# Kernel optimization log

Measured on AMD Instinct MI355X. Metric: run time of the kernel, lower is better.

## Reference

```python
import jax, jax.numpy as jnp
import numpy as np

B, T, D, H, L = 8192, 80, 32, 64, 3


def setup_inputs() -> dict:
    key = jax.random.key(0)
    ks = jax.random.split(key, 16)
    s = lambda k, shape, fan: jax.random.normal(k, shape, jnp.float32) / np.sqrt(fan)
    inp = {"x": jax.random.normal(ks[0], (B, T, D), jnp.float32)}
    dims_in = [D, H, H]
    i = 1
    for l in range(L):
        din = dims_in[l]
        inp[f"W_ih{l}"] = s(ks[i], (H, din), H); i += 1
        inp[f"W_hh{l}"] = s(ks[i], (H, H), H); i += 1
        inp[f"b_ih{l}"] = s(ks[i], (H,), H); i += 1
        inp[f"b_hh{l}"] = s(ks[i], (H,), H); i += 1
    inp["W_fc"] = s(ks[i], (1, H), H); i += 1
    inp["b_fc"] = s(ks[i], (1,), H)
    return inp


def _rnn_layer(xs, W_ih, W_hh, b_ih, b_hh):
    # xs: [T, B, Din] -> ys: [T, B, H]; tanh RNN recurrence (PyTorch nn.RNN math)
    pre = jnp.einsum('tbd,hd->tbh', xs, W_ih) + b_ih + b_hh  # input proj precomputed
    h0 = jnp.zeros((xs.shape[1], W_hh.shape[0]), xs.dtype)
    def step(h, p):
        h_new = jnp.tanh(p + h @ W_hh.T)
        return h_new, h_new
    _, ys = jax.lax.scan(step, h0, pre)
    return ys


def reference(x, W_ih0, W_hh0, b_ih0, b_hh0, W_ih1, W_hh1, b_ih1, b_hh1,
              W_ih2, W_hh2, b_ih2, b_hh2, W_fc, b_fc):
    # x: [B, T, D] (batch_first) -> time-major [T, B, D]
    h = jnp.swapaxes(x, 0, 1)
    params = [(W_ih0, W_hh0, b_ih0, b_hh0),
              (W_ih1, W_hh1, b_ih1, b_hh1),
              (W_ih2, W_hh2, b_ih2, b_hh2)]
    for (W_ih, W_hh, b_ih, b_hh) in params:
        h = _rnn_layer(h, W_ih, W_hh, b_ih, b_hh)
    last = h[-1]                      # [B, H] == out[:, -1, :]
    return last @ W_fc.T + b_fc       # [B, 1]
```

## Files before the change

### kernel.cpp

```cpp
#include <hip/hip_runtime.h>
#include <hip/hip_bf16.h>
#include <cstddef>


typedef __attribute__((ext_vector_type(8))) short s16x8;
typedef __attribute__((ext_vector_type(4))) short s16x4;
typedef __attribute__((ext_vector_type(4))) float fx4;

#define MFMA32(A, B, C) __builtin_amdgcn_mfma_f32_16x16x32_bf16((A), (B), (C), 0, 0, 0)

#if __has_builtin(__builtin_amdgcn_exp2f)
#define EXP2F(x) __builtin_amdgcn_exp2f(x)
#else
#define EXP2F(x) exp2f(x)
#endif
#if __has_builtin(__builtin_amdgcn_rcpf)
#define RCPF(x) __builtin_amdgcn_rcpf(x)
#else
#define RCPF(x) (1.0f / (x))
#endif

static constexpr float K2LOG2E = 2.8853900817779268f;

__device__ __forceinline__ short f2bf(float f) {
  union { float f; unsigned u; } v; v.f = f;
  unsigned r = v.u + 0x7FFFu + ((v.u >> 16) & 1u);
  return (short)(r >> 16);
}
__device__ __forceinline__ float bf2f(short s) {
  union { unsigned u; float f; } v; v.u = ((unsigned)(unsigned short)s) << 16;
  return v.f;
}
__device__ __forceinline__ unsigned pk2bf(float a, float b) {
  float2 t; t.x = a; t.y = b;
  union { __hip_bfloat162 h; unsigned u; } c;
  c.h = __float22bfloat162_rn(t);
  return c.u;
}

__device__ __forceinline__ s16x8 wfragA32(const float* W, int ncols, int row, int col0) {
  const float* p = W + row * ncols + col0;
  s16x8 r;
#pragma unroll
  for (int i = 0; i < 8; ++i) r[i] = f2bf(p[i]);
  return r;
}

__device__ __forceinline__ s16x8 wfragWhh32(const float* W, int row, int q, int h) {
  const float* p = W + row * 64 + 32 * h + 4 * q;
  s16x8 r;
#pragma unroll
  for (int i = 0; i < 4; ++i) r[i] = f2bf(p[i]);
#pragma unroll
  for (int i = 0; i < 4; ++i) r[4 + i] = f2bf(p[16 + i]);
  return r;
}

__device__ __forceinline__ s16x4 tanh_pack(fx4 acc, const float* bs) {
  float h[4];
#pragma unroll
  for (int r = 0; r < 4; ++r) {
    float e = EXP2F(__builtin_fmaf(acc[r], K2LOG2E, bs[r]));
    h[r] = __builtin_fmaf(-2.f, RCPF(e + 1.f), 1.f);
  }
  union { unsigned u[2]; s16x4 v; } p;
  p.u[0] = pk2bf(h[0], h[1]);
  p.u[1] = pk2bf(h[2], h[3]);
  return p.v;
}

union U8 { s16x8 v; s16x4 h[2]; };

__global__ __launch_bounds__(192, 2) void rnn3_chunk4(
    const float* __restrict__ x,
    const float* __restrict__ Wih0, const float* __restrict__ Whh0,
    const float* __restrict__ bih0, const float* __restrict__ bhh0,
    const float* __restrict__ Wih1, const float* __restrict__ Whh1,
    const float* __restrict__ bih1, const float* __restrict__ bhh1,
    const float* __restrict__ Wih2, const float* __restrict__ Whh2,
    const float* __restrict__ bih2, const float* __restrict__ bhh2,
    const float* __restrict__ Wfc, const float* __restrict__ bfc,
    float* __restrict__ out)
{
  __shared__ __align__(16) short hb[2][8][16][72];

  const int tid = threadIdx.x;
  const int wv  = __builtin_amdgcn_readfirstlane(tid >> 6);
  const int ln  = tid & 63;
  const int q   = ln >> 4;
  const int m15 = ln & 15;
  const int bbase = (int)blockIdx.x * 16;

  const float* Wih = (wv == 0) ? Wih0 : (wv == 1) ? Wih1 : Wih2;
  const float* Whh = (wv == 0) ? Whh0 : (wv == 1) ? Whh1 : Whh2;
  const float* bi  = (wv == 0) ? bih0 : (wv == 1) ? bih1 : bih2;
  const float* bh  = (wv == 0) ? bhh0 : (wv == 1) ? bhh1 : bhh2;
  const int kin = (wv == 0) ? 32 : 64;

  s16x8 wiA[4], wiB[4];
  s16x8 wh32[4][2];
  const s16x8 z8 = {0, 0, 0, 0, 0, 0, 0, 0};
#pragma unroll
  for (int t4 = 0; t4 < 4; ++t4) {
    const int row = 16 * t4 + m15;
    wiA[t4] = wfragA32(Wih, kin, row, 8 * q);
    wiB[t4] = wv ? wfragA32(Wih, 64, row, 32 + 8 * q) : z8;
    wh32[t4][0] = wfragWhh32(Whh, row, q, 0);
    wh32[t4][1] = wfragWhh32(Whh, row, q, 1);
  }

  float bsc[4][4];
#pragma unroll
  for (int t4 = 0; t4 < 4; ++t4)
#pragma unroll
    for (int r = 0; r < 4; ++r) {
      const int j = 16 * t4 + 4 * q + r;
      bsc[t4][r] = (bi[j] + bh[j]) * K2LOG2E;
    }

  const fx4 z4 = {0.f, 0.f, 0.f, 0.f};
  U8 hA, hB;
  hA.v = z8; hB.v = z8;

  const float* xr = x + (size_t)(bbase + m15) * (80 * 32) + 8 * q;
  fx4 xb0[4], xb1[4];
  if (wv == 0) {
#pragma unroll
    for (int jj = 0; jj < 4; ++jj) {
      xb0[jj] = *(const fx4*)(xr + jj * 32);
      xb1[jj] = *(const fx4*)(xr + jj * 32 + 4);
    }
  }

  for (int m = 0; m < 22; ++m) {
    const int lt0 = 4 * (m - wv);
    if (0 <= lt0 && lt0 <= 76) {
      s16x8 inA[4], inB[4];
      if (wv == 0) {
#pragma unroll
        for (int jj = 0; jj < 4; ++jj) {
          union { unsigned u[4]; s16x8 v; } xp;
          xp.u[0] = pk2bf(xb0[jj][0], xb0[jj][1]);
          xp.u[1] = pk2bf(xb0[jj][2], xb0[jj][3]);
          xp.u[2] = pk2bf(xb1[jj][0], xb1[jj][1]);
          xp.u[3] = pk2bf(xb1[jj][2], xb1[jj][3]);
          inA[jj] = xp.v; inB[jj] = z8;
        }
#pragma unroll
        for (int jj = 0; jj < 4; ++jj) {
          const int tt = (lt0 + 4 + jj <= 79) ? lt0 + 4 + jj : 79;
          xb0[jj] = *(const fx4*)(xr + tt * 32);
          xb1[jj] = *(const fx4*)(xr + tt * 32 + 4);
        }
      } else {
#pragma unroll
        for (int jj = 0; jj < 4; ++jj) {
          const short* up = &hb[wv - 1][(lt0 + jj) & 7][m15][8 * q];
          inA[jj] = *(const s16x8*)(up);
          inB[jj] = *(const s16x8*)(up + 32);
        }
      }
#pragma unroll
      for (int jj = 0; jj < 4; ++jj) {
        const int st = (lt0 + jj) & 7;
        fx4 acc[4];
#pragma unroll
        for (int t4 = 0; t4 < 4; ++t4) acc[t4] = MFMA32(wiA[t4], inA[jj], z4);
        if (wv) {
#pragma unroll
          for (int t4 = 0; t4 < 4; ++t4) acc[t4] = MFMA32(wiB[t4], inB[jj], acc[t4]);
        }
#pragma unroll
        for (int t4 = 0; t4 < 4; ++t4) acc[t4] = MFMA32(wh32[t4][0], hA.v, acc[t4]);
#pragma unroll
        for (int t4 = 0; t4 < 4; ++t4) acc[t4] = MFMA32(wh32[t4][1], hB.v, acc[t4]);
        U8 nA, nB;
#pragma unroll
        for (int t4 = 0; t4 < 4; ++t4) {
          s16x4 hv = tanh_pack(acc[t4], bsc[t4]);
          if (t4 < 2) nA.h[t4] = hv; else nB.h[t4 - 2] = hv;
          if (wv < 2) {
            *(s16x4*)(&hb[wv][st][m15][4 * q + 16 * t4]) = hv;
          }
        }
        hA = nA; hB = nB;
      }
    }
    __syncthreads();
  }

  if (wv == 2) {
    float sv = 0.f;
#pragma unroll
    for (int kf = 0; kf < 4; ++kf) {
      const s16x4 hh = (kf < 2) ? hA.h[kf] : hB.h[kf - 2];
#pragma unroll
      for (int i = 0; i < 4; ++i)
        sv += bf2f(hh[i]) * Wfc[16 * kf + 4 * q + i];
    }
    sv += __shfl_xor(sv, 16, 64);
    sv += __shfl_xor(sv, 32, 64);
    if (ln < 16) out[bbase + ln] = sv + bfc[0];
  }
}

extern "C" void kernel_launch(void* const* d_in, const int* in_sizes, int n_in,
                              void* d_out, int out_size, void* d_ws, size_t ws_size,
                              hipStream_t stream) {
  const float* x    = (const float*)d_in[0];
  const float* Wih0 = (const float*)d_in[1];
  const float* Whh0 = (const float*)d_in[2];
  const float* bih0 = (const float*)d_in[3];
  const float* bhh0 = (const float*)d_in[4];
  const float* Wih1 = (const float*)d_in[5];
  const float* Whh1 = (const float*)d_in[6];
  const float* bih1 = (const float*)d_in[7];
  const float* bhh1 = (const float*)d_in[8];
  const float* Wih2 = (const float*)d_in[9];
  const float* Whh2 = (const float*)d_in[10];
  const float* bih2 = (const float*)d_in[11];
  const float* bhh2 = (const float*)d_in[12];
  const float* Wfc  = (const float*)d_in[13];
  const float* bfc  = (const float*)d_in[14];

  rnn3_chunk4<<<dim3(512), dim3(192), 0, stream>>>(
      x, Wih0, Whh0, bih0, bhh0, Wih1, Whh1, bih1, bhh1,
      Wih2, Whh2, bih2, bhh2, Wfc, bfc, (float*)d_out);
}
```

Measured before the change: 187.0 us.

## Process two interleaved 16-row batch tiles per block to hide MFMA latency

Result: slower. 214.6 us (+14.8%).

```diff
diff --git a/kernel.cpp b/kernel.cpp
--- a/kernel.cpp
+++ b/kernel.cpp
@@ -56,6 +56,17 @@
   return r;
 }
 
+__device__ __forceinline__ s16x8 load_pack_x(const float* p) {
+  fx4 a = *(const fx4*)(p);
+  fx4 b = *(const fx4*)(p + 4);
+  union { unsigned u[4]; s16x8 v; } xp;
+  xp.u[0] = pk2bf(a[0], a[1]);
+  xp.u[1] = pk2bf(a[2], a[3]);
+  xp.u[2] = pk2bf(b[0], b[1]);
+  xp.u[3] = pk2bf(b[2], b[3]);
+  return xp.v;
+}
+
 __device__ __forceinline__ s16x4 tanh_pack(fx4 acc, const float* bs) {
   float h[4];
 #pragma unroll
@@ -71,7 +82,7 @@
 
 union U8 { s16x8 v; s16x4 h[2]; };
 
-__global__ __launch_bounds__(192, 2) void rnn3_chunk4(
+__global__ __launch_bounds__(192, 1) void rnn3_dual(
     const float* __restrict__ x,
     const float* __restrict__ Wih0, const float* __restrict__ Whh0,
     const float* __restrict__ bih0, const float* __restrict__ bhh0,
@@ -82,14 +93,14 @@
     const float* __restrict__ Wfc, const float* __restrict__ bfc,
     float* __restrict__ out)
 {
-  __shared__ __align__(16) short hb[2][8][16][72];
+  __shared__ __align__(16) short hb[2][8][32][72];
 
   const int tid = threadIdx.x;
   const int wv  = __builtin_amdgcn_readfirstlane(tid >> 6);
   const int ln  = tid & 63;
   const int q   = ln >> 4;
   const int m15 = ln & 15;
-  const int bbase = (int)blockIdx.x * 16;
+  const int bbase = (int)blockIdx.x * 32;
 
   const float* Wih = (wv == 0) ? Wih0 : (wv == 1) ? Wih1 : Wih2;
   const float* Whh = (wv == 0) ? Whh0 : (wv == 1) ? Whh1 : Whh2;
@@ -119,88 +130,112 @@
     }
 
   const fx4 z4 = {0.f, 0.f, 0.f, 0.f};
-  U8 hA, hB;
-  hA.v = z8; hB.v = z8;
-
-  const float* xr = x + (size_t)(bbase + m15) * (80 * 32) + 8 * q;
-  fx4 xb0[4], xb1[4];
+  U8 hA[2], hB[2];
+  hA[0].v = z8; hB[0].v = z8; hA[1].v = z8; hB[1].v = z8;
+
+  const float* xr0 = x + (size_t)(bbase + m15) * (80 * 32) + 8 * q;
+  const float* xr1 = x + (size_t)(bbase + 16 + m15) * (80 * 32) + 8 * q;
+  s16x8 xin[2][4];
   if (wv == 0) {
 #pragma unroll
     for (int jj = 0; jj < 4; ++jj) {
-      xb0[jj] = *(const fx4*)(xr + jj * 32);
-      xb1[jj] = *(const fx4*)(xr + jj * 32 + 4);
+      xin[0][jj] = load_pack_x(xr0 + jj * 32);
+      xin[1][jj] = load_pack_x(xr1 + jj * 32);
     }
   }
 
   for (int m = 0; m < 22; ++m) {
     const int lt0 = 4 * (m - wv);
     if (0 <= lt0 && lt0 <= 76) {
-      s16x8 inA[4], inB[4];
+      s16x8 inA[2][4], inB[2][4];
       if (wv == 0) {
 #pragma unroll
-        for (int jj = 0; jj < 4; ++jj) {
-          union { unsigned u[4]; s16x8 v; } xp;
-          xp.u[0] = pk2bf(xb0[jj][0], xb0[jj][1]);
-          xp.u[1] = pk2bf(xb0[jj][2], xb0[jj][3]);
-          xp.u[2] = pk2bf(xb1[jj][0], xb1[jj][1]);
-          xp.u[3] = pk2bf(xb1[jj][2], xb1[jj][3]);
-          inA[jj] = xp.v; inB[jj] = z8;
-        }
+        for (int u = 0; u < 2; ++u)
+#pragma unroll
+          for (int jj = 0; jj < 4; ++jj) {
+            inA[u][jj] = xin[u][jj];
+            inB[u][jj] = z8;
+          }
 #pragma unroll
         for (int jj = 0; jj < 4; ++jj) {
           const int tt = (lt0 + 4 + jj <= 79) ? lt0 + 4 + jj : 79;
-          xb0[jj] = *(const fx4*)(xr + tt * 32);
-          xb1[jj] = *(const fx4*)(xr + tt * 32 + 4);
+          xin[0][jj] = load_pack_x(xr0 + tt * 32);
+          xin[1][jj] = load_pack_x(xr1 + tt * 32);
         }
       } else {
 #pragma unroll
-        for (int jj = 0; jj < 4; ++jj) {
-          const short* up = &hb[wv - 1][(lt0 + jj) & 7][m15][8 * q];
-          inA[jj] = *(const s16x8*)(up);
-          inB[jj] = *(const s16x8*)(up + 32);
+        for (int u = 0; u < 2; ++u)
+#pragma unroll
+          for (int jj = 0; jj < 4; ++jj) {
+            const short* up = &hb[wv - 1][(lt0 + jj) & 7][16 * u + m15][8 * q];
+            inA[u][jj] = *(const s16x8*)(up);
+            inB[u][jj] = *(const s16x8*)(up + 32);
+          }
+      }
+#pragma unroll
+      for (int jj = 0; jj < 4; ++jj) {
+        const int st = (lt0 + jj) & 7;
+        fx4 acc[2][4];
+#pragma unroll
+        for (int t4 = 0; t4 < 4; ++t4)
+#pragma unroll
+          for (int u = 0; u < 2; ++u)
+            acc[u][t4] = MFMA32(wiA[t4], inA[u][jj], z4);
+        if (wv) {
+#pragma unroll
+          for (int t4 = 0; t4 < 4; ++t4)
+#pragma unroll
+            for (int u = 0; u < 2; ++u)
+              acc[u][t4] = MFMA32(wiB[t4], inB[u][jj], acc[u][t4]);
+        }
+#pragma unroll
+        for (int t4 = 0; t4 < 4; ++t4)
+#pragma unroll
+          for (int u = 0; u < 2; ++u)
+            acc[u][t4] = MFMA32(wh32[t4][0], hA[u].v, acc[u][t4]);
+#pragma unroll
+        for (int t4 = 0; t4 < 4; ++t4)
+#pragma unroll
+          for (int u = 0; u < 2; ++u)
+            acc[u][t4] = MFMA32(wh32[t4][1], hB[u].v, acc[u][t4]);
+#pragma unroll
+        for (int u = 0; u < 2; ++u) {
+          U8 nA, nB;
+#pragma unroll
+          for (int t4 = 0; t4 < 4; ++t4) {
+            s16x4 hv = tanh_pack(acc[u][t4], bsc[t4]);
+            if (t4 < 2) nA.h[t4] = hv; else nB.h[t4 - 2] = hv;
+            if (wv < 2) {
+              *(s16x4*)(&hb[wv][st][16 * u + m15][4 * q + 16 * t4]) = hv;
+            }
+          }
+          hA[u] = nA; hB[u] = nB;
         }
       }
-#pragma unroll
-      for (int jj = 0; jj < 4; ++jj) {
-        const int st = (lt0 + jj) & 7;
-        fx4 acc[4];
-#pragma unroll
-        for (int t4 = 0; t4 < 4; ++t4) acc[t4] = MFMA32(wiA[t4], inA[jj], z4);
-        if (wv) {
-#pragma unroll
-          for (int t4 = 0; t4 < 4; ++t4) acc[t4] = MFMA32(wiB[t4], inB[jj], acc[t4]);
-        }
-#pragma unroll
-        for (int t4 = 0; t4 < 4; ++t4) acc[t4] = MFMA32(wh32[t4][0], hA.v, acc[t4]);
-#pragma unroll
-        for (int t4 = 0; t4 < 4; ++t4) acc[t4] = MFMA32(wh32[t4][1], hB.v, acc[t4]);
-        U8 nA, nB;
-#pragma unroll
-        for (int t4 = 0; t4 < 4; ++t4) {
-          s16x4 hv = tanh_pack(acc[t4], bsc[t4]);
-          if (t4 < 2) nA.h[t4] = hv; else nB.h[t4 - 2] = hv;
-          if (wv < 2) {
-            *(s16x4*)(&hb[wv][st][m15][4 * q + 16 * t4]) = hv;
-          }
-        }
-        hA = nA; hB = nB;
+    }
+    __syncthreads();
+  }
+
+  if (wv == 2) {
+    float svs[2];
+#pragma unroll
+    for (int u = 0; u < 2; ++u) {
+      float sv = 0.f;
+#pragma unroll
+      for (int kf = 0; kf < 4; ++kf) {
+        const s16x4 hh = (kf < 2) ? hA[u].h[kf] : hB[u].h[kf - 2];
+#pragma unroll
+        for (int i = 0; i < 4; ++i)
+          sv += bf2f(hh[i]) * Wfc[16 * kf + 4 * q + i];
       }
-    }
-    __syncthreads();
-  }
-
-  if (wv == 2) {
-    float sv = 0.f;
-#pragma unroll
-    for (int kf = 0; kf < 4; ++kf) {
-      const s16x4 hh = (kf < 2) ? hA.h[kf] : hB.h[kf - 2];
-#pragma unroll
-      for (int i = 0; i < 4; ++i)
-        sv += bf2f(hh[i]) * Wfc[16 * kf + 4 * q + i];
-    }
-    sv += __shfl_xor(sv, 16, 64);
-    sv += __shfl_xor(sv, 32, 64);
-    if (ln < 16) out[bbase + ln] = sv + bfc[0];
+      sv += __shfl_xor(sv, 16, 64);
+      sv += __shfl_xor(sv, 32, 64);
+      svs[u] = sv;
+    }
+    if (ln < 16) {
+      out[bbase + ln]      = svs[0] + bfc[0];
+      out[bbase + 16 + ln] = svs[1] + bfc[0];
+    }
   }
 }
 
@@ -223,7 +258,7 @@
   const float* Wfc  = (const float*)d_in[13];
   const float* bfc  = (const float*)d_in[14];
 
-  rnn3_chunk4<<<dim3(512), dim3(192), 0, stream>>>(
+  rnn3_dual<<<dim3(256), dim3(192), 0, stream>>>(
       x, Wih0, Whh0, bih0, bhh0, Wih1, Whh1, bih1, bhh1,
       Wih2, Whh2, bih2, bhh2, Wfc, bfc, (float*)d_out);
 }
```
